# Kernel tuning notes

Hardware: AMD Instinct MI355X
Metric: run time of the kernel (lower is better)

Reference implementation:

```python
import jax, jax.numpy as jnp
import numpy as np

# norse LIFParameters defaults with v_th overridden to 0.23
DT = 1e-3
TAU_SYN_INV = 200.0   # 1/5e-3
TAU_MEM_INV = 100.0   # 1/1e-2
V_TH = 0.23
ENC_V_TH = 1.0        # encoder uses default LIFParameters (v_th=1.0)
SEQ_LEN = 24
HIDDEN = 256
N_CLASSES = 10


def heaviside(x):
    return (x > 0).astype(x.dtype)


def encode(x):
    """ConstantCurrentLIFEncoder: lif_current_encoder over SEQ_LEN steps. x: [B, F] -> [T, B, F] spikes."""
    def step(v, _):
        v = v + DT * TAU_MEM_INV * (x - v)          # dv = dt*tau_mem_inv*((v_leak - v) + I)
        z = heaviside(v - ENC_V_TH)
        v = (1.0 - z) * v                            # reset to v_reset = 0
        return v, z
    _, zs = jax.lax.scan(step, jnp.zeros_like(x), None, length=SEQ_LEN)
    return zs


def lif_ff_step(inp, v, i):
    """norse lif_feed_forward_step: decay v with old i, decay i, spike, reset, then add input to i."""
    v_dec = v + DT * TAU_MEM_INV * (i - v)           # v_leak = 0
    i_dec = i * (1.0 - DT * TAU_SYN_INV)
    z = heaviside(v_dec - V_TH)
    v_new = (1.0 - z) * v_dec                        # v_reset = 0
    i_new = i_dec + inp
    return z, v_new, i_new


def setup_inputs() -> dict:
    key = jax.random.key(0)
    ks = jax.random.split(key, 8)
    B, F = 4096, 1024
    def lin(k, fan_in, fan_out):
        bound = 1.0 / np.sqrt(fan_in)
        kw, kb = jax.random.split(k)
        W = jax.random.uniform(kw, (fan_out, fan_in), jnp.float32, -bound, bound)
        b = jax.random.uniform(kb, (fan_out,), jnp.float32, -bound, bound)
        return W, b
    x = jax.random.normal(ks[0], (B, F), jnp.float32)
    W1, b1 = lin(ks[1], F, HIDDEN)
    W2, b2 = lin(ks[2], HIDDEN, HIDDEN)
    W3, b3 = lin(ks[3], HIDDEN, HIDDEN)
    Wli = jax.random.normal(ks[4], (N_CLASSES, HIDDEN), jnp.float32) * np.sqrt(2.0 / HIDDEN)
    return {"x": x, "W1": W1, "b1": b1, "W2": W2, "b2": b2, "W3": W3, "b3": b3, "Wli": Wli}


def reference(x, W1, b1, W2, b2, W3, b3, Wli):
    # dropout layers are identity in eval mode
    enc = encode(x)                                   # [T, B, F]
    B = x.shape[0]
    z2 = lambda d: jnp.zeros((B, d), x.dtype)
    carry0 = (z2(HIDDEN), z2(HIDDEN), z2(HIDDEN), z2(HIDDEN), z2(HIDDEN), z2(HIDDEN),
              z2(N_CLASSES), z2(N_CLASSES))
    def step(c, z):
        v1, i1, v2, i2, v3, i3, vo, io = c
        o1, v1, i1 = lif_ff_step(z @ W1.T + b1, v1, i1)
        o2, v2, i2 = lif_ff_step(o1 @ W2.T + b2, v2, i2)
        o2 = o2 + o1                                  # residual
        o3, v3, i3 = lif_ff_step(o2 @ W3.T + b3, v3, i3)
        o3 = o3 + o2                                  # residual
        # LILinearCell li_step: v from old i, i decays then accumulates W @ input (no bias)
        vo = vo + DT * TAU_MEM_INV * (io - vo)
        io = io * (1.0 - DT * TAU_SYN_INV) + o3 @ Wli.T
        return (v1, i1, v2, i2, v3, i3, vo, io), vo
    _, voltages = jax.lax.scan(step, carry0, enc)     # [T, B, n_classes]
    return voltages[-1]                               # decode = last timestep
```

## Files before the change

### kernel.cpp

```cpp
#include <hip/hip_runtime.h>
#include <hip/hip_bf16.h>

#define FEAT   1024
#define HID    256
#define TSTEPS 24
#define NCLS   10

typedef unsigned int u32;
typedef unsigned long long u64;
typedef unsigned short u16;
typedef float v2f __attribute__((ext_vector_type(2)));

constexpr int OFF_W1T  = 0;
constexpr int OFF_W2T  = OFF_W1T + 1025*HID;
constexpr int OFF_W3T  = OFF_W2T + 257*HID;
constexpr int OFF_WLI  = OFF_W3T + 257*HID;
constexpr int OFF_B1   = OFF_WLI + NCLS*HID;
constexpr int OFF_B2   = OFF_B1 + HID;
constexpr int OFF_B3   = OFF_B2 + HID;

struct CoefT { float c[TSTEPS]; };
constexpr CoefT make_coef() {
    CoefT r{};
    double c = 0.0, p9 = 1.0;
    r.c[TSTEPS-1] = 0.0f;
    for (int u = TSTEPS-1; u > 0; u--) {
        c = 0.8 * c + 0.1 * p9;
        p9 *= 0.9;
        r.c[u-1] = (float)c;
    }
    return r;
}
__device__ constexpr CoefT COEF = make_coef();

__device__ __forceinline__ u32 rfl(u32 v) {
    return (u32)__builtin_amdgcn_readfirstlane((int)v);
}

__device__ __forceinline__ u32 detect_bf16(const void* __restrict__ x, u32 lane) {
    float v = __bfloat162float(((const __hip_bfloat16*)x)[lane]);
    u64 bad = __ballot(!(fabsf(v) < 100.0f));
    return bad == 0ull ? 1u : 0u;
}

__device__ __forceinline__ float rd_any(const void* p, int idx, u32 isbf) {
    return isbf ? __bfloat162float(((const __hip_bfloat16*)p)[idx])
                : ((const float*)p)[idx];
}

__device__ __forceinline__ float4 rd4(const void* p, int i, u32 isbf) {
    if (isbf) {
        const u32* q = (const u32*)p;
        u32 a = q[i >> 1], b = q[(i >> 1) + 1];
        float4 r;
        r.x = __uint_as_float(a << 16); r.y = __uint_as_float(a & 0xffff0000u);
        r.z = __uint_as_float(b << 16); r.w = __uint_as_float(b & 0xffff0000u);
        return r;
    }
    return ((const float4*)p)[i >> 2];
}

__global__ __launch_bounds__(256) void prep_k(const void* __restrict__ x,
        const void* W1, const void* W2, const void* W3, const void* Wli,
        const void* b1, const void* b2, const void* b3, float* __restrict__ ws) {
    const u32 isbf = detect_bf16(x, threadIdx.x & 63);
    const u32 t = threadIdx.x;
    int b = blockIdx.x;

    if (b == 384) {
        for (u32 e = t; e < NCLS*HID; e += 256) ws[OFF_WLI + e] = rd_any(Wli, e, isbf);
        ws[OFF_B1 + t] = rd_any(b1, t, isbf);
        ws[OFF_B2 + t] = rd_any(b2, t, isbf);
        ws[OFF_B3 + t] = rd_any(b3, t, isbf);
        ws[OFF_W1T + 1024*HID + t] = 0.f;
        ws[OFF_W2T + 256*HID + t] = 0.f;
        ws[OFF_W3T + 256*HID + t] = 0.f;
        return;
    }

    const void* src; float* dst; int srcW, h0, f0;
    if (b < 256)      { src = W1; dst = ws + OFF_W1T; srcW = FEAT; h0 = (b >> 5) * 32; f0 = (b & 31) * 32; }
    else if (b < 320) { int tb = b - 256; src = W2; dst = ws + OFF_W2T; srcW = HID; h0 = (tb >> 3) * 32; f0 = (tb & 7) * 32; }
    else              { int tb = b - 320; src = W3; dst = ws + OFF_W3T; srcW = HID; h0 = (tb >> 3) * 32; f0 = (tb & 7) * 32; }

    __shared__ float sm[32 * 36];
    {
        u32 r = t >> 3, c4 = (t & 7) * 4;
        float4 w = rd4(src, (h0 + r) * srcW + f0 + c4, isbf);
        *(float4*)&sm[r * 36 + c4] = w;
    }
    __syncthreads();
    {
        u32 f = t >> 3, h4 = (t & 7) * 4;
        float4 o;
        o.x = sm[(h4 + 0) * 36 + f];
        o.y = sm[(h4 + 1) * 36 + f];
        o.z = sm[(h4 + 2) * 36 + f];
        o.w = sm[(h4 + 3) * 36 + f];
        *(float4*)&dst[(size_t)(f0 + f) * HID + h0 + h4] = o;
    }
}

__device__ __forceinline__ u32 mbcnt64(u64 m) {
    return __builtin_amdgcn_mbcnt_hi((u32)(m >> 32),
           __builtin_amdgcn_mbcnt_lo((u32)m, 0u));
}


__device__ __forceinline__ u32 build_listE(u16* list, u32 lm, u32 lane) {
    u32 cnt = (u32)__builtin_popcount(lm);
    u32 pos = 0, n = 0;
    #pragma unroll
    for (int b = 0; b < 5; b++) {
        u64 B = __ballot(((cnt >> b) & 1u) != 0);
        pos += mbcnt64(B) << b;
        n += ((u32)__builtin_popcountll(B)) << b;
    }
    while (lm) {
        u32 j = (u32)__builtin_ctz(lm); lm &= lm - 1;
        list[pos++] = (u16)((lane << 4) + j);
    }
    u32 np = (n + 1u) & ~1u;
    if (lane == 0 && np != n) list[n] = (u16)1024;
    return np;
}

__device__ __forceinline__ u32 build_listZ(u16* list, u32 lm, u32 start, u32 lane) {
    u32 cnt = (u32)__builtin_popcount(lm);
    u64 B0 = __ballot((cnt & 1u) != 0);
    u64 B1 = __ballot((cnt & 2u) != 0);
    u64 B2 = __ballot((cnt & 4u) != 0);
    u32 pos = start + mbcnt64(B0) + 2u*mbcnt64(B1) + 4u*mbcnt64(B2);
    u32 n = start + (u32)__builtin_popcountll(B0) + 2u*(u32)__builtin_popcountll(B1)
          + 4u*(u32)__builtin_popcountll(B2);
    while (lm) {
        u32 j = (u32)__builtin_ctz(lm); lm &= lm - 1;
        list[pos++] = (u16)((lane << 2) + j);
    }
    u32 np = (n + 1u) & ~1u;
    if (lane == 0 && np != n) list[n] = (u16)256;
    return np;
}

#define GADD(AA, BB, V) do { AA += (v2f){(V).x, (V).y}; BB += (v2f){(V).z, (V).w}; } while (0)

__device__ __forceinline__ void gather(v2f& A, v2f& B, const float* __restrict__ Wt,
                                       const u16* __restrict__ list, u32 np, u32 lane16) {
    const char* __restrict__ base = (const char*)Wt;
    u32 c = 0;
    for (; c + 8 <= np; c += 8) {
        uint4 d = *(const uint4*)(list + c);
        u32 w0 = rfl(d.x), w1 = rfl(d.y), w2 = rfl(d.z), w3 = rfl(d.w);
        const float4 v0 = *(const float4*)(base + ((w0 & 0xffffu) << 10) + lane16);
        const float4 v1 = *(const float4*)(base + ((w0 >> 16)     << 10) + lane16);
        const float4 v2 = *(const float4*)(base + ((w1 & 0xffffu) << 10) + lane16);
        const float4 v3 = *(const float4*)(base + ((w1 >> 16)     << 10) + lane16);
        const float4 v4 = *(const float4*)(base + ((w2 & 0xffffu) << 10) + lane16);
        const float4 v5 = *(const float4*)(base + ((w2 >> 16)     << 10) + lane16);
        const float4 v6 = *(const float4*)(base + ((w3 & 0xffffu) << 10) + lane16);
        const float4 v7 = *(const float4*)(base + ((w3 >> 16)     << 10) + lane16);
        GADD(A, B, v0); GADD(A, B, v1); GADD(A, B, v2); GADD(A, B, v3);
        GADD(A, B, v4); GADD(A, B, v5); GADD(A, B, v6); GADD(A, B, v7);
    }
    for (; c < np; c += 2) {
        u32 d = rfl(*(const u32*)(list + c));
        const float4 v0 = *(const float4*)(base + ((d & 0xffffu) << 10) + lane16);
        const float4 v1 = *(const float4*)(base + ((d >> 16)     << 10) + lane16);
        GADD(A, B, v0); GADD(A, B, v1);
    }
}

__device__ __forceinline__ void gather_dual(v2f& A2, v2f& B2, v2f& A3, v2f& B3,
        const float* __restrict__ W2t, const float* __restrict__ W3t,
        const u16* __restrict__ list, u32 np, u32 lane16) {
    const char* __restrict__ p2 = (const char*)W2t;
    const char* __restrict__ p3 = (const char*)W3t;
    u32 c = 0;
    for (; c + 4 <= np; c += 4) {
        uint2 d = *(const uint2*)(list + c);
        u32 w0 = rfl(d.x), w1 = rfl(d.y);
        u32 o0 = (w0 & 0xffffu) << 10, o1 = (w0 >> 16) << 10;
        u32 o2 = (w1 & 0xffffu) << 10, o3 = (w1 >> 16) << 10;
        const float4 a0 = *(const float4*)(p2 + o0 + lane16);
        const float4 a1 = *(const float4*)(p2 + o1 + lane16);
        const float4 a2 = *(const float4*)(p2 + o2 + lane16);
        const float4 a3 = *(const float4*)(p2 + o3 + lane16);
        const float4 c0 = *(const float4*)(p3 + o0 + lane16);
        const float4 c1 = *(const float4*)(p3 + o1 + lane16);
        const float4 c2 = *(const float4*)(p3 + o2 + lane16);
        const float4 c3 = *(const float4*)(p3 + o3 + lane16);
        GADD(A2, B2, a0); GADD(A2, B2, a1); GADD(A2, B2, a2); GADD(A2, B2, a3);
        GADD(A3, B3, c0); GADD(A3, B3, c1); GADD(A3, B3, c2); GADD(A3, B3, c3);
    }
    for (; c < np; c += 2) {
        u32 d = rfl(*(const u32*)(list + c));
        u32 o0 = (d & 0xffffu) << 10, o1 = (d >> 16) << 10;
        const float4 a0 = *(const float4*)(p2 + o0 + lane16);
        const float4 a1 = *(const float4*)(p2 + o1 + lane16);
        const float4 c0 = *(const float4*)(p3 + o0 + lane16);
        const float4 c1 = *(const float4*)(p3 + o1 + lane16);
        GADD(A2, B2, a0); GADD(A2, B2, a1);
        GADD(A3, B3, c0); GADD(A3, B3, c1);
    }
}

__global__ __launch_bounds__(128, 4) void snn_k(const void* __restrict__ xin,
                                                const float* __restrict__ ws,
                                                void* __restrict__ out,
                                                int batch) {
    const u32 tid  = threadIdx.x;
    const u32 w    = tid >> 6;
    const u32 lane = tid & 63;
    const int row  = blockIdx.x * 2 + (int)w;
    if (row >= batch) return;
    const u32 lane16 = lane * 16;
    const u32 isbf = detect_bf16(xin, lane);

    const float* __restrict__ W1T = ws + OFF_W1T;
    const float* __restrict__ W2T = ws + OFF_W2T;
    const float* __restrict__ W3T = ws + OFF_W3T;
    const float* __restrict__ WLI = ws + OFF_WLI;

    __shared__ u32 sched[2][12 * 64];
    __shared__ __align__(16) u16 lst[2][1024];
    u16* const lE = lst[w];
    u16* const lL = lst[w];

    {
        float xv[16];
        if (isbf) {
            const uint4* xp = (const uint4*)((const u16*)xin + (size_t)row*FEAT + lane*16);
            uint4 A = xp[0], B = xp[1];
            u32 wd[8] = {A.x, A.y, A.z, A.w, B.x, B.y, B.z, B.w};
            #pragma unroll
            for (int i = 0; i < 8; i++) {
                xv[2*i]   = __uint_as_float(wd[i] << 16);
                xv[2*i+1] = __uint_as_float(wd[i] & 0xffff0000u);
            }
        } else {
            const float4* xp = (const float4*)((const float*)xin + (size_t)row*FEAT + lane*16);
            float4 A = xp[0], B = xp[1], C = xp[2], D = xp[3];
            float tmp[16] = {A.x,A.y,A.z,A.w,B.x,B.y,B.z,B.w,C.x,C.y,C.z,C.w,D.x,D.y,D.z,D.w};
            #pragma unroll
            for (int i = 0; i < 16; i++) xv[i] = tmp[i];
        }
        u32 smreg[12];
        #pragma unroll
        for (int i = 0; i < 12; i++) smreg[i] = 0;
        #pragma unroll
        for (int j = 0; j < 16; j++) {
            float v = 0.f;
            #pragma unroll
            for (int t = 0; t < TSTEPS; t++) {
                v = v + 0.1f * (xv[j] - v);
                bool z = v > 1.0f;
                v = z ? 0.0f : v;
                if (z) smreg[t >> 1] |= 1u << (((t & 1) << 4) + j);
            }
        }
        #pragma unroll
        for (int i = 0; i < 12; i++) sched[w][i * 64 + lane] = smreg[i];
    }

    float v1[4], i1[4], v2[4], i2[4], v3[4], i3[4], g[4];
    #pragma unroll
    for (int k = 0; k < 4; k++) {
        v1[k]=0.f; i1[k]=0.f; v2[k]=0.f; i2[k]=0.f; v3[k]=0.f; i3[k]=0.f; g[k]=0.f;
    }
    const u32 lane4 = lane * 4;
    const float4 b1v = *(const float4*)(ws + OFF_B1 + lane4);
    const float4 b2v = *(const float4*)(ws + OFF_B2 + lane4);
    const float4 b3v = *(const float4*)(ws + OFF_B3 + lane4);

    u32 pairreg = 0;
    for (int t = 0; t < TSTEPS; t++) {
        if ((t & 1) == 0) pairreg = sched[w][(t >> 1) * 64 + lane];
        const u32 lmE = (t & 1) ? (pairreg >> 16) : (pairreg & 0xffffu);

        v2f accA = {b1v.x, b1v.y}, accB = {b1v.z, b1v.w};
        if (__ballot(lmE != 0u)) {
            u32 npE = build_listE(lE, lmE, lane);
            gather(accA, accB, W1T, lE, npE, lane16);
        }
        float a1[4] = {accA.x, accA.y, accB.x, accB.y};

        float o1v[4]; u32 lm1 = 0;
        #pragma unroll
        for (int kk = 0; kk < 4; kk++) {
            float vd = v1[kk] + 0.1f * (i1[kk] - v1[kk]);
            i1[kk] = i1[kk] * 0.8f;
            bool z = vd > 0.23f;
            v1[kk] = z ? 0.0f : vd;
            i1[kk] = i1[kk] + a1[kk];
            o1v[kk] = z ? 1.0f : 0.0f;
            lm1 |= (z ? 1u : 0u) << kk;
        }

        v2f acc2A = {b2v.x, b2v.y}, acc2B = {b2v.z, b2v.w};
        v2f acc3A = {b3v.x, b3v.y}, acc3B = {b3v.z, b3v.w};
        u32 np1 = 0;
        if (__ballot(lm1 != 0u)) {
            np1 = build_listZ(lL, lm1, 0u, lane);
            gather_dual(acc2A, acc2B, acc3A, acc3B, W2T, W3T, lL, np1, lane16);
        }
        float a2[4] = {acc2A.x, acc2A.y, acc2B.x, acc2B.y};

        float o2v[4]; u32 lm2 = 0;
        #pragma unroll
        for (int kk = 0; kk < 4; kk++) {
            float vd = v2[kk] + 0.1f * (i2[kk] - v2[kk]);
            i2[kk] = i2[kk] * 0.8f;
            bool z = vd > 0.23f;
            v2[kk] = z ? 0.0f : vd;
            i2[kk] = i2[kk] + a2[kk];
            o2v[kk] = (z ? 1.0f : 0.0f) + o1v[kk];
            lm2 |= (z ? 1u : 0u) << kk;
        }

        if (__ballot(lm2 != 0u)) {
            u32 np2 = build_listZ(lL, lm2, np1, lane);
            gather(acc3A, acc3B, W3T, lL + np1, np2 - np1, lane16);
        }
        float a3[4] = {acc3A.x, acc3A.y, acc3B.x, acc3B.y};

        const float cf = COEF.c[t];
        #pragma unroll
        for (int kk = 0; kk < 4; kk++) {
            float vd = v3[kk] + 0.1f * (i3[kk] - v3[kk]);
            i3[kk] = i3[kk] * 0.8f;
            bool z = vd > 0.23f;
            v3[kk] = z ? 0.0f : vd;
            i3[kk] = i3[kk] + a3[kk];
            float o3 = (z ? 1.0f : 0.0f) + o2v[kk];
            g[kk] += cf * o3;
        }
    }

    float s[NCLS];
    #pragma unroll
    for (int c = 0; c < NCLS; c++) {
        const float4 wv = *(const float4*)(WLI + c*HID + lane4);
        float p = g[0]*wv.x + g[1]*wv.y + g[2]*wv.z + g[3]*wv.w;
        #pragma unroll
        for (int d = 32; d > 0; d >>= 1) p += __shfl_xor(p, d, 64);
        s[c] = p;
    }
    if (lane == 0) {
        if (isbf) {
            __hip_bfloat16* o = (__hip_bfloat16*)out + (size_t)row*NCLS;
            #pragma unroll
            for (int c = 0; c < NCLS; c++) o[c] = __float2bfloat16(s[c]);
        } else {
            float* o = (float*)out + (size_t)row*NCLS;
            #pragma unroll
            for (int c = 0; c < NCLS; c++) o[c] = s[c];
        }
    }
}

extern "C" void kernel_launch(void* const* d_in, const int* in_sizes, int n_in,
                              void* d_out, int out_size, void* d_ws, size_t ws_size,
                              hipStream_t stream) {
    const void* x   = d_in[0];
    const void* W1  = d_in[1];
    const void* b1  = d_in[2];
    const void* W2  = d_in[3];
    const void* b2  = d_in[4];
    const void* W3  = d_in[5];
    const void* b3  = d_in[6];
    const void* Wli = d_in[7];
    float* ws = (float*)d_ws;
    const int batch = in_sizes[0] / FEAT;

    prep_k<<<385, 256, 0, stream>>>(x, W1, W2, W3, Wli, b1, b2, b3, ws);
    snn_k<<<(batch + 1) / 2, 128, 0, stream>>>(x, ws, d_out, batch);
}
```

Baseline: 144.4 us.

## Precompute layer-1 sums for periodic encoder spike patterns

```diff
diff --git a/kernel.cpp b/kernel.cpp
--- a/kernel.cpp
+++ b/kernel.cpp
@@ -32,6 +32,17 @@
     return r;
 }
 __device__ constexpr CoefT COEF = make_coef();
+
+__device__ const unsigned char DIVTAB[TSTEPS] = {
+    0, 0, 0, 1, 2, 4, 8, 17,
+    0, 2, 0, 5, 0, 8, 2, 17,
+    0, 4, 0, 3, 8, 0, 0, 21
+};
+#define PMASK4 0x00888888u
+#define PMASK5 0x00084210u
+#define PMASK6 0x00820820u
+#define PMASK7 0x00102040u
+#define PMASK8 0x00808080u
 
 __device__ __forceinline__ u32 rfl(u32 v) {
     return (u32)__builtin_amdgcn_readfirstlane((int)v);
@@ -222,10 +233,14 @@
     const float* __restrict__ WLI = ws + OFF_WLI;
 
     __shared__ u32 sched[2][12 * 64];
-    __shared__ __align__(16) u16 lst[2][1024];
+    __shared__ __align__(16) u16 lst[2][768];
+    __shared__ float4 Ucls[2][5][64];
     u16* const lE = lst[w];
     u16* const lL = lst[w];
 
+    u32 clsm[5];
+    #pragma unroll
+    for (int i = 0; i < 5; i++) clsm[i] = 0;
     {
         float xv[16];
         if (isbf) {
@@ -250,16 +265,39 @@
         #pragma unroll
         for (int j = 0; j < 16; j++) {
             float v = 0.f;
+            u32 fm = 0;
             #pragma unroll
             for (int t = 0; t < TSTEPS; t++) {
                 v = v + 0.1f * (xv[j] - v);
                 bool z = v > 1.0f;
                 v = z ? 0.0f : v;
-                if (z) smreg[t >> 1] |= 1u << (((t & 1) << 4) + j);
+                fm |= (z ? 1u : 0u) << t;
             }
+            if      (fm == PMASK4) clsm[0] |= 1u << j;
+            else if (fm == PMASK5) clsm[1] |= 1u << j;
+            else if (fm == PMASK6) clsm[2] |= 1u << j;
+            else if (fm == PMASK7) clsm[3] |= 1u << j;
+            else if (fm == PMASK8) clsm[4] |= 1u << j;
+            else if (fm) {
+                #pragma unroll
+                for (int i = 0; i < 12; i++) {
+                    u32 b = (fm >> (2*i)) & 3u;
+                    smreg[i] |= ((b & 1u) << j) | ((b >> 1) << (16 + j));
+                }
+            }
         }
         #pragma unroll
         for (int i = 0; i < 12; i++) sched[w][i * 64 + lane] = smreg[i];
+    }
+
+    #pragma unroll
+    for (int i = 0; i < 5; i++) {
+        v2f A = {0.f, 0.f}, B = {0.f, 0.f};
+        if (__ballot(clsm[i] != 0u)) {
+            u32 np = build_listE(lE, clsm[i], lane);
+            gather(A, B, W1T, lE, np, lane16);
+        }
+        Ucls[w][i][lane] = make_float4(A.x, A.y, B.x, B.y);
     }
 
     float v1[4], i1[4], v2[4], i2[4], v3[4], i3[4], g[4];
@@ -278,6 +316,12 @@
         const u32 lmE = (t & 1) ? (pairreg >> 16) : (pairreg & 0xffffu);
 
         v2f accA = {b1v.x, b1v.y}, accB = {b1v.z, b1v.w};
+        u32 dv = DIVTAB[t];
+        while (dv) {
+            u32 i = (u32)__builtin_ctz(dv); dv &= dv - 1u;
+            float4 u = Ucls[w][i][lane];
+            accA += (v2f){u.x, u.y}; accB += (v2f){u.z, u.w};
+        }
         if (__ballot(lmE != 0u)) {
             u32 npE = build_listE(lE, lmE, lane);
             gather(accA, accB, W1T, lE, npE, lane16);
```

Result: no change. 146.3 us (+1.4%).
